# Performance work log

Measured on AMD Instinct MI355X. Metric: run time of the kernel, lower is better.

## Reference

```python
import jax, jax.numpy as jnp
import numpy as np

B, N, E = 4, 512, 128
NODE_F, EDGE_F, DYN_F, L = 16, 8, 6, 3
TOT_F = NODE_F + DYN_F  # 22


def setup_inputs() -> dict:
    key = jax.random.key(0)
    ks = jax.random.split(key, 20)
    s = 0.05
    return {
        "node_features": jax.random.normal(ks[0], (B, N, NODE_F), jnp.float32),
        "edge_features": jax.random.normal(ks[1], (B, N, N, EDGE_F), jnp.float32),
        "W": jax.random.normal(ks[2], (B, N, N), jnp.float32),
        "assigned": jax.random.randint(ks[3], (B, N), 0, 2) > 0,
        "open_group": jax.random.randint(ks[4], (B, N), 0, 2) > 0,
        "action_mask": jax.random.randint(ks[5], (B, N), 0, 2) > 0,
        "build_limit": jax.random.uniform(ks[6], (B, 3), jnp.float32, 0.5, 2.0),
        "open_group_size": jax.random.uniform(ks[7], (B, 3), jnp.float32, 0.0, 2.0),
        "node_embed_w": jax.random.normal(ks[8], (TOT_F, E), jnp.float32) * s,
        "node_embed_b": jnp.zeros((E,), jnp.float32),
        "mp_node_w": jax.random.normal(ks[9], (L, E, E), jnp.float32) * s,
        "mp_edge_w": jax.random.normal(ks[10], (L, EDGE_F, E), jnp.float32) * s,
        "mp_weight_w": jax.random.normal(ks[11], (L, E), jnp.float32) * s,
        "mp_out_w": jax.random.normal(ks[12], (L, E, E), jnp.float32) * s,
        "mp_out_b": jnp.zeros((L, E), jnp.float32),
        "context_w": jax.random.normal(ks[13], (E, E), jnp.float32) * s,
        "key_w": jax.random.normal(ks[14], (E, E), jnp.float32) * s,
        "logit_bias": jnp.zeros((1,), jnp.float32),
    }


def _policy_logits(node_features, edge_features, W, build_limit, open_group_size,
                   node_embed_w, node_embed_b, mp_node_w, mp_edge_w, mp_weight_w,
                   mp_out_w, mp_out_b, context_w, key_w, logit_bias,
                   assigned, open_group, action_mask):
    # --- dynamic node features: [B,N,6] ---
    ratio = open_group_size / jnp.maximum(build_limit, 1e-6)  # [B,3]
    dyn = jnp.concatenate([
        assigned.astype(jnp.float32)[..., None],
        open_group.astype(jnp.float32)[..., None],
        action_mask.astype(jnp.float32)[..., None],
        jnp.broadcast_to(ratio[:, None, :], (node_features.shape[0], node_features.shape[1], 3)),
    ], axis=-1)
    x = jnp.concatenate([node_features, dyn], axis=-1)  # [B,N,22]
    h = x @ node_embed_w + node_embed_b  # [B,N,E]

    # --- edge-aware message passing, residual per layer ---
    for l in range(L):
        hi = h @ mp_node_w[l]  # [B,N,E]
        ej = jnp.einsum('bijf,fe->bije', edge_features, mp_edge_w[l])  # [B,N,N,E]
        wij = W[..., None] * mp_weight_w[l]  # [B,N,N,E]
        msg = jnp.tanh(hi[:, :, None, :] + ej + wij)  # [B,N,N,E]
        agg = msg.mean(axis=2)  # [B,N,E]
        h = h + agg @ mp_out_w[l] + mp_out_b[l]

    # --- context attention logits ---
    og = open_group.astype(jnp.float32)
    has_open = jnp.any(open_group, axis=-1, keepdims=True)  # [B,1]
    denom = jnp.maximum(og.sum(axis=-1, keepdims=True), 1.0)  # [B,1]
    group_mean = (h * og[..., None]).sum(axis=1) / denom  # [B,E]
    sep_emb = h[:, 0, :]
    context = jnp.where(has_open, group_mean, sep_emb)  # [B,E]
    query = context @ context_w  # [B,E]
    keys = h @ key_w  # [B,N,E]
    logits = jnp.einsum('be,bne->bn', query, keys) / jnp.sqrt(jnp.float32(h.shape[-1]))
    logits = logits + logit_bias[0]
    logits = jnp.where(action_mask, logits, -1e9)
    return logits


def reference(node_features, edge_features, W, assigned, open_group, action_mask,
              build_limit, open_group_size, node_embed_w, node_embed_b,
              mp_node_w, mp_edge_w, mp_weight_w, mp_out_w, mp_out_b,
              context_w, key_w, logit_bias):
    return _policy_logits(node_features, edge_features, W, build_limit, open_group_size,
                          node_embed_w, node_embed_b, mp_node_w, mp_edge_w, mp_weight_w,
                          mp_out_w, mp_out_b, context_w, key_w, logit_bias,
                          assigned, open_group, action_mask)
```

## Files before the change

kernel.cpp:

```cpp
#include <hip/hip_runtime.h>
#include <math.h>

#define BB 4
#define NN 512
#define EE 128
#define NODE_F 16
#define EDGE_F 8
#define LL 3

typedef __attribute__((ext_vector_type(8))) short bf16x8;
typedef __attribute__((ext_vector_type(4))) float f32x4;

__device__ __forceinline__ ushort bf_hi(float x) {
    uint u = __float_as_uint(x);
    return (ushort)((u + 0x7fffu + ((u >> 16) & 1u)) >> 16);
}
__device__ __forceinline__ float bf_f(ushort h) {
    return __uint_as_float(((uint)h) << 16);
}

__global__ __launch_bounds__(512) void k_rows(
    const float* __restrict__ nf,
    const float* __restrict__ ef,
    const float* __restrict__ W,
    const int*   __restrict__ assigned,
    const int*   __restrict__ open_group,
    const int*   __restrict__ action_mask,
    const float* __restrict__ build_limit,
    const float* __restrict__ open_group_size,
    const float* __restrict__ embed_w,
    const float* __restrict__ embed_b,
    const float* __restrict__ node_w,
    const float* __restrict__ edge_w,
    const float* __restrict__ weight_w,
    const float* __restrict__ out_w,
    const float* __restrict__ out_b,
    float* __restrict__ hout)
{
    const int i   = blockIdx.x;
    const int b   = blockIdx.y;
    const int t   = threadIdx.x;
    const int l   = t & 63;
    const int w   = t >> 6;
    const int e   = t & 127;
    const int ks  = t >> 7;
    const int row = b * NN + i;

    __shared__ bf16x8 afr[32 * 64];
    __shared__ float hsh[EE];
    __shared__ float hipart[4][EE];
    __shared__ float opart[4][EE];
    __shared__ float aggfin[EE];
    __shared__ float xsh[24];

    if (t < NODE_F) {
        xsh[t] = nf[row * NODE_F + t];
    } else if (t == 16) {
        xsh[16] = assigned[row] ? 1.0f : 0.0f;
    } else if (t == 17) {
        xsh[17] = open_group[row] ? 1.0f : 0.0f;
    } else if (t == 18) {
        xsh[18] = action_mask[row] ? 1.0f : 0.0f;
    } else if (t < 22) {
        int k = t - 19;
        xsh[t] = open_group_size[b * 3 + k] / fmaxf(build_limit[b * 3 + k], 1e-6f);
    }

    {
        const float* efr = ef + (size_t)row * NN * EDGE_F;
        const float* Wr  = W + (size_t)row * NN;
        #pragma unroll
        for (int q = 0; q < 4; ++q) {
            const int eid = t + 512 * q;
            const int ll  = eid & 63;
            const int jt  = eid >> 6;
            const int g   = ll >> 4;
            const int jj  = jt * 16 + (ll & 15);
            bf16x8 frag;
            if (g < 3) {
                const float4 a = *(const float4*)&efr[jj * 8];
                const float4 c4 = *(const float4*)&efr[jj * 8 + 4];
                float v[8] = {a.x, a.y, a.z, a.w, c4.x, c4.y, c4.z, c4.w};
                if (g < 2) {
                    #pragma unroll
                    for (int m = 0; m < 8; ++m) frag[m] = (short)bf_hi(v[m]);
                } else {
                    #pragma unroll
                    for (int m = 0; m < 8; ++m) {
                        ushort h = bf_hi(v[m]);
                        frag[m] = (short)bf_hi(v[m] - bf_f(h));
                    }
                }
            } else {
                float wv = Wr[jj];
                ushort h = bf_hi(wv);
                ushort lo = bf_hi(wv - bf_f(h));
                frag = (bf16x8){(short)h, (short)h, (short)lo, 0, 0, 0, 0, 0};
            }
            afr[eid] = frag;
        }
    }
    __syncthreads();

    if (t < EE) {
        float h0 = embed_b[t];
        #pragma unroll
        for (int k = 0; k < 22; ++k)
            h0 = fmaf(xsh[k], embed_w[k * EE + t], h0);
        hsh[t] = h0;
    }

    const float c  = 2.8853900817779268f;
    const int  le  = l & 15;
    const int  g   = l >> 4;
    const int  eN  = w * 16 + le;

    for (int lay = 0; lay < LL; ++lay) {
        __syncthreads();

        {
            const float* nw = node_w + lay * EE * EE + ks * 32 * EE + e;
            float hp = 0.0f;
            #pragma unroll
            for (int kk = 0; kk < 2; ++kk) {
                float wreg[16];
                #pragma unroll
                for (int k2 = 0; k2 < 16; ++k2)
                    wreg[k2] = nw[(kk * 16 + k2) * EE];
                #pragma unroll
                for (int k2 = 0; k2 < 16; ++k2)
                    hp = fmaf(hsh[ks * 32 + kk * 16 + k2], wreg[k2], hp);
            }
            hipart[ks][e] = hp;
        }

        bf16x8 bfrag;
        if (g == 3) {
            float x = c * weight_w[lay * EE + eN];
            ushort h = bf_hi(x);
            ushort lo = bf_hi(x - bf_f(h));
            bfrag = (bf16x8){(short)h, (short)lo, (short)h, 0, 0, 0, 0, 0};
        } else {
            const float* ewp = edge_w + lay * EDGE_F * EE + eN;
            if (g == 1) {
                #pragma unroll
                for (int m = 0; m < 8; ++m) {
                    float x = c * ewp[m * EE];
                    ushort h = bf_hi(x);
                    bfrag[m] = (short)bf_hi(x - bf_f(h));
                }
            } else {
                #pragma unroll
                for (int m = 0; m < 8; ++m)
                    bfrag[m] = (short)bf_hi(c * ewp[m * EE]);
            }
        }
        __syncthreads();

        const float hq = c * ((hipart[0][eN] + hipart[1][eN])
                            + (hipart[2][eN] + hipart[3][eN]));
        const f32x4 cin = {hq, hq, hq, hq};

        f32x4 rsum = {0.0f, 0.0f, 0.0f, 0.0f};
        #pragma unroll 4
        for (int jt = 0; jt < 32; ++jt) {
            bf16x8 a = afr[jt * 64 + l];
            f32x4 acc = __builtin_amdgcn_mfma_f32_16x16x32_bf16(a, bfrag, cin, 0, 0, 0);
            #pragma unroll
            for (int r = 0; r < 4; ++r) {
                float ex = __builtin_amdgcn_exp2f(acc[r]);
                rsum[r] += __builtin_amdgcn_rcpf(ex + 1.0f);
            }
        }
        float s = (rsum[0] + rsum[1]) + (rsum[2] + rsum[3]);
        s += __shfl_xor(s, 16);
        s += __shfl_xor(s, 32);
        if (l < 16)
            aggfin[w * 16 + le] = 1.0f - s * (1.0f / 256.0f);
        __syncthreads();

        {
            const float* ow = out_w + lay * EE * EE + ks * 32 * EE + e;
            float op = 0.0f;
            #pragma unroll
            for (int kk = 0; kk < 2; ++kk) {
                float wreg[16];
                #pragma unroll
                for (int k2 = 0; k2 < 16; ++k2)
                    wreg[k2] = ow[(kk * 16 + k2) * EE];
                #pragma unroll
                for (int k2 = 0; k2 < 16; ++k2)
                    op = fmaf(aggfin[ks * 32 + kk * 16 + k2], wreg[k2], op);
            }
            opart[ks][e] = op;
        }
        __syncthreads();

        if (t < EE) {
            hsh[t] = hsh[t] + out_b[lay * EE + t]
                   + (opart[0][t] + opart[1][t]) + (opart[2][t] + opart[3][t]);
        }
    }

    __syncthreads();
    if (t < EE) hout[(size_t)row * EE + t] = hsh[t];
}

__global__ __launch_bounds__(1024) void k_ctx(
    const float* __restrict__ hbuf,
    const int*   __restrict__ open_group,
    const float* __restrict__ context_w,
    const float* __restrict__ key_w,
    float* __restrict__ qk)
{
    const int b = blockIdx.x;
    const int t = threadIdx.x;
    const int e = t & 127;
    const int s = t >> 7;

    __shared__ float gmsh[8][EE];
    __shared__ float cntsh[8];
    __shared__ float csh[EE];
    __shared__ float qsh[EE];

    const float* hb = hbuf + (size_t)b * NN * EE;

    float gm = 0.0f, cnt = 0.0f;
    const int n0 = s * 64;
    #pragma unroll 8
    for (int u = 0; u < 64; ++u) {
        const int n = n0 + u;
        const float m = (float)open_group[b * NN + n];
        gm = fmaf(m, hb[(size_t)n * EE + e], gm);
        cnt += m;
    }
    gmsh[s][e] = gm;
    if (e == 0) cntsh[s] = cnt;
    __syncthreads();

    if (s == 0) {
        float ca = 0.0f, ga = 0.0f;
        #pragma unroll
        for (int u = 0; u < 8; ++u) { ca += cntsh[u]; ga += gmsh[u][e]; }
        csh[e] = (ca > 0.0f) ? (ga / fmaxf(ca, 1.0f)) : hb[e];
    }
    __syncthreads();

    if (s == 0) {
        float q = 0.0f;
        #pragma unroll
        for (int kk = 0; kk < 8; ++kk) {
            float wreg[16];
            #pragma unroll
            for (int k2 = 0; k2 < 16; ++k2)
                wreg[k2] = context_w[(kk * 16 + k2) * EE + e];
            #pragma unroll
            for (int k2 = 0; k2 < 16; ++k2)
                q = fmaf(csh[kk * 16 + k2], wreg[k2], q);
        }
        qsh[e] = q;
    }
    __syncthreads();

    if (s == 0) {
        float acc = 0.0f;
        const float* kr = key_w + e * EE;
        #pragma unroll
        for (int kk = 0; kk < 8; ++kk) {
            float wreg[16];
            #pragma unroll
            for (int k2 = 0; k2 < 16; ++k2)
                wreg[k2] = kr[kk * 16 + k2];
            #pragma unroll
            for (int k2 = 0; k2 < 16; ++k2)
                acc = fmaf(wreg[k2], qsh[kk * 16 + k2], acc);
        }
        qk[b * EE + e] = acc;
    }
}

__global__ __launch_bounds__(512) void k_logits(
    const float* __restrict__ hbuf,
    const float* __restrict__ qk,
    const int*   __restrict__ action_mask,
    const float* __restrict__ logit_bias,
    float* __restrict__ out)
{
    const int b    = blockIdx.y;
    const int base = blockIdx.x * 32;
    const int wid  = threadIdx.x >> 6;
    const int lane = threadIdx.x & 63;

    const float* hb = hbuf + (size_t)b * NN * EE;
    const float* qb = qk + b * EE;
    const float q0 = qb[lane];
    const float q1 = qb[lane + 64];
    const float lb = logit_bias[0];

    #pragma unroll
    for (int u = 0; u < 4; ++u) {
        const int r = base + wid * 4 + u;
        const float* hr = hb + (size_t)r * EE;
        float p = hr[lane] * q0 + hr[lane + 64] * q1;
        #pragma unroll
        for (int off = 32; off; off >>= 1)
            p += __shfl_down(p, off);
        if (lane == 0) {
            float v = fmaf(p, 0.08838834764831845f, lb);
            out[b * NN + r] = action_mask[b * NN + r] ? v : -1000000000.0f;
        }
    }
}

extern "C" void kernel_launch(void* const* d_in, const int* in_sizes, int n_in,
                              void* d_out, int out_size, void* d_ws, size_t ws_size,
                              hipStream_t stream) {
    const float* nf         = (const float*)d_in[0];
    const float* ef         = (const float*)d_in[1];
    const float* W          = (const float*)d_in[2];
    const int*   assigned   = (const int*)d_in[3];
    const int*   open_group = (const int*)d_in[4];
    const int*   action_mask= (const int*)d_in[5];
    const float* build_limit= (const float*)d_in[6];
    const float* og_size    = (const float*)d_in[7];
    const float* embed_w    = (const float*)d_in[8];
    const float* embed_b    = (const float*)d_in[9];
    const float* node_w     = (const float*)d_in[10];
    const float* edge_w     = (const float*)d_in[11];
    const float* weight_w   = (const float*)d_in[12];
    const float* out_w      = (const float*)d_in[13];
    const float* out_b      = (const float*)d_in[14];
    const float* context_w  = (const float*)d_in[15];
    const float* key_w      = (const float*)d_in[16];
    const float* logit_bias = (const float*)d_in[17];

    float* hbuf = (float*)d_ws;
    float* qk   = hbuf + (size_t)BB * NN * EE;

    dim3 grid_rows(NN, BB, 1);
    k_rows<<<grid_rows, 512, 0, stream>>>(nf, ef, W, assigned, open_group,
        action_mask, build_limit, og_size, embed_w, embed_b, node_w, edge_w,
        weight_w, out_w, out_b, hbuf);

    k_ctx<<<BB, 1024, 0, stream>>>(hbuf, open_group, context_w, key_w, qk);

    dim3 grid_log(16, BB, 1);
    k_logits<<<grid_log, 512, 0, stream>>>(hbuf, qk, action_mask, logit_bias,
        (float*)d_out);
}
```

Baseline: 231.7 us.

## Replace shared-memory partial sums with wave shuffles and fuse group-mean via atomics

Inside k_rows, the per-layer node and out projections are remapped so each wave reduces its K-slices with xor shuffles instead of writing partials to shared memory. This removes two block-wide barriers per layer. The open-group mean is now accumulated with global atomics at the end of k_rows, so k_ctx shrinks to a 128-thread kernel that no longer rescans hbuf. A small zeroing kernel is added for the accumulators. Float atomics make the group sum order nondeterministic, and the new layout changes how the weight reads coalesce.

```diff
diff --git a/kernel.cpp b/kernel.cpp
--- a/kernel.cpp
+++ b/kernel.cpp
@@ -17,6 +17,11 @@
 }
 __device__ __forceinline__ float bf_f(ushort h) {
     return __uint_as_float(((uint)h) << 16);
+}
+
+__global__ __launch_bounds__(512) void k_zero(float* __restrict__ gbuf) {
+    for (int i = threadIdx.x; i < BB * EE + BB; i += 512)
+        gbuf[i] = 0.0f;
 }
 
 __global__ __launch_bounds__(512) void k_rows(
@@ -35,21 +40,19 @@
     const float* __restrict__ weight_w,
     const float* __restrict__ out_w,
     const float* __restrict__ out_b,
-    float* __restrict__ hout)
+    float* __restrict__ hout,
+    float* __restrict__ gsum,
+    float* __restrict__ gcnt)
 {
     const int i   = blockIdx.x;
     const int b   = blockIdx.y;
     const int t   = threadIdx.x;
     const int l   = t & 63;
     const int w   = t >> 6;
-    const int e   = t & 127;
-    const int ks  = t >> 7;
     const int row = b * NN + i;
 
     __shared__ bf16x8 afr[32 * 64];
     __shared__ float hsh[EE];
-    __shared__ float hipart[4][EE];
-    __shared__ float opart[4][EE];
     __shared__ float aggfin[EE];
     __shared__ float xsh[24];
 
@@ -118,9 +121,9 @@
     for (int lay = 0; lay < LL; ++lay) {
         __syncthreads();
 
+        float hp = 0.0f;
         {
-            const float* nw = node_w + lay * EE * EE + ks * 32 * EE + e;
-            float hp = 0.0f;
+            const float* nw = node_w + lay * EE * EE + g * 32 * EE + eN;
             #pragma unroll
             for (int kk = 0; kk < 2; ++kk) {
                 float wreg[16];
@@ -129,10 +132,12 @@
                     wreg[k2] = nw[(kk * 16 + k2) * EE];
                 #pragma unroll
                 for (int k2 = 0; k2 < 16; ++k2)
-                    hp = fmaf(hsh[ks * 32 + kk * 16 + k2], wreg[k2], hp);
-            }
-            hipart[ks][e] = hp;
-        }
+                    hp = fmaf(hsh[g * 32 + kk * 16 + k2], wreg[k2], hp);
+            }
+            hp += __shfl_xor(hp, 16);
+            hp += __shfl_xor(hp, 32);
+        }
+        const float hq = c * hp;
 
         bf16x8 bfrag;
         if (g == 3) {
@@ -155,10 +160,7 @@
                     bfrag[m] = (short)bf_hi(c * ewp[m * EE]);
             }
         }
-        __syncthreads();
-
-        const float hq = c * ((hipart[0][eN] + hipart[1][eN])
-                            + (hipart[2][eN] + hipart[3][eN]));
+
         const f32x4 cin = {hq, hq, hq, hq};
 
         f32x4 rsum = {0.0f, 0.0f, 0.0f, 0.0f};
@@ -176,12 +178,12 @@
         s += __shfl_xor(s, 16);
         s += __shfl_xor(s, 32);
         if (l < 16)
-            aggfin[w * 16 + le] = 1.0f - s * (1.0f / 256.0f);
+            aggfin[eN] = 1.0f - s * (1.0f / 256.0f);
         __syncthreads();
 
+        float op = 0.0f;
         {
-            const float* ow = out_w + lay * EE * EE + ks * 32 * EE + e;
-            float op = 0.0f;
+            const float* ow = out_w + lay * EE * EE + g * 32 * EE + eN;
             #pragma unroll
             for (int kk = 0; kk < 2; ++kk) {
                 float wreg[16];
@@ -190,93 +192,71 @@
                     wreg[k2] = ow[(kk * 16 + k2) * EE];
                 #pragma unroll
                 for (int k2 = 0; k2 < 16; ++k2)
-                    op = fmaf(aggfin[ks * 32 + kk * 16 + k2], wreg[k2], op);
-            }
-            opart[ks][e] = op;
-        }
-        __syncthreads();
-
-        if (t < EE) {
-            hsh[t] = hsh[t] + out_b[lay * EE + t]
-                   + (opart[0][t] + opart[1][t]) + (opart[2][t] + opart[3][t]);
-        }
+                    op = fmaf(aggfin[g * 32 + kk * 16 + k2], wreg[k2], op);
+            }
+            op += __shfl_xor(op, 16);
+            op += __shfl_xor(op, 32);
+        }
+        if (l < 16)
+            hsh[eN] = hsh[eN] + out_b[lay * EE + eN] + op;
     }
 
     __syncthreads();
-    if (t < EE) hout[(size_t)row * EE + t] = hsh[t];
-}
-
-__global__ __launch_bounds__(1024) void k_ctx(
+    if (t < EE) {
+        const float hv = hsh[t];
+        hout[(size_t)row * EE + t] = hv;
+        if (open_group[row]) atomicAdd(&gsum[b * EE + t], hv);
+    }
+    if (t == 256 && open_group[row]) atomicAdd(&gcnt[b], 1.0f);
+}
+
+__global__ __launch_bounds__(128) void k_ctx(
     const float* __restrict__ hbuf,
-    const int*   __restrict__ open_group,
+    const float* __restrict__ gsum,
+    const float* __restrict__ gcnt,
     const float* __restrict__ context_w,
     const float* __restrict__ key_w,
     float* __restrict__ qk)
 {
     const int b = blockIdx.x;
-    const int t = threadIdx.x;
-    const int e = t & 127;
-    const int s = t >> 7;
-
-    __shared__ float gmsh[8][EE];
-    __shared__ float cntsh[8];
+    const int e = threadIdx.x;
+
     __shared__ float csh[EE];
     __shared__ float qsh[EE];
 
-    const float* hb = hbuf + (size_t)b * NN * EE;
-
-    float gm = 0.0f, cnt = 0.0f;
-    const int n0 = s * 64;
-    #pragma unroll 8
-    for (int u = 0; u < 64; ++u) {
-        const int n = n0 + u;
-        const float m = (float)open_group[b * NN + n];
-        gm = fmaf(m, hb[(size_t)n * EE + e], gm);
-        cnt += m;
-    }
-    gmsh[s][e] = gm;
-    if (e == 0) cntsh[s] = cnt;
+    const float cnt = gcnt[b];
+    const float ctx = (cnt > 0.0f) ? (gsum[b * EE + e] / fmaxf(cnt, 1.0f))
+                                   : hbuf[(size_t)b * NN * EE + e];
+    csh[e] = ctx;
     __syncthreads();
 
-    if (s == 0) {
-        float ca = 0.0f, ga = 0.0f;
-        #pragma unroll
-        for (int u = 0; u < 8; ++u) { ca += cntsh[u]; ga += gmsh[u][e]; }
-        csh[e] = (ca > 0.0f) ? (ga / fmaxf(ca, 1.0f)) : hb[e];
-    }
+    float q = 0.0f;
+    #pragma unroll
+    for (int kk = 0; kk < 8; ++kk) {
+        float wreg[16];
+        #pragma unroll
+        for (int k2 = 0; k2 < 16; ++k2)
+            wreg[k2] = context_w[(kk * 16 + k2) * EE + e];
+        #pragma unroll
+        for (int k2 = 0; k2 < 16; ++k2)
+            q = fmaf(csh[kk * 16 + k2], wreg[k2], q);
+    }
+    qsh[e] = q;
     __syncthreads();
 
-    if (s == 0) {
-        float q = 0.0f;
-        #pragma unroll
-        for (int kk = 0; kk < 8; ++kk) {
-            float wreg[16];
-            #pragma unroll
-            for (int k2 = 0; k2 < 16; ++k2)
-                wreg[k2] = context_w[(kk * 16 + k2) * EE + e];
-            #pragma unroll
-            for (int k2 = 0; k2 < 16; ++k2)
-                q = fmaf(csh[kk * 16 + k2], wreg[k2], q);
-        }
-        qsh[e] = q;
-    }
-    __syncthreads();
-
-    if (s == 0) {
-        float acc = 0.0f;
-        const float* kr = key_w + e * EE;
-        #pragma unroll
-        for (int kk = 0; kk < 8; ++kk) {
-            float wreg[16];
-            #pragma unroll
-            for (int k2 = 0; k2 < 16; ++k2)
-                wreg[k2] = kr[kk * 16 + k2];
-            #pragma unroll
-            for (int k2 = 0; k2 < 16; ++k2)
-                acc = fmaf(wreg[k2], qsh[kk * 16 + k2], acc);
-        }
-        qk[b * EE + e] = acc;
-    }
+    float acc = 0.0f;
+    const float* kr = key_w + e * EE;
+    #pragma unroll
+    for (int kk = 0; kk < 8; ++kk) {
+        float wreg[16];
+        #pragma unroll
+        for (int k2 = 0; k2 < 16; ++k2)
+            wreg[k2] = kr[kk * 16 + k2];
+        #pragma unroll
+        for (int k2 = 0; k2 < 16; ++k2)
+            acc = fmaf(wreg[k2], qsh[kk * 16 + k2], acc);
+    }
+    qk[b * EE + e] = acc;
 }
 
 __global__ __launch_bounds__(512) void k_logits(
@@ -336,13 +316,18 @@
 
     float* hbuf = (float*)d_ws;
     float* qk   = hbuf + (size_t)BB * NN * EE;
+    float* gbuf = qk + BB * EE;
+    float* gsum = gbuf;
+    float* gcnt = gbuf + BB * EE;
+
+    k_zero<<<1, 512, 0, stream>>>(gbuf);
 
     dim3 grid_rows(NN, BB, 1);
     k_rows<<<grid_rows, 512, 0, stream>>>(nf, ef, W, assigned, open_group,
         action_mask, build_limit, og_size, embed_w, embed_b, node_w, edge_w,
-        weight_w, out_w, out_b, hbuf);
-
-    k_ctx<<<BB, 1024, 0, stream>>>(hbuf, open_group, context_w, key_w, qk);
+        weight_w, out_w, out_b, hbuf, gsum, gcnt);
+
+    k_ctx<<<BB, 128, 0, stream>>>(hbuf, gsum, gcnt, context_w, key_w, qk);
 
     dim3 grid_log(16, BB, 1);
     k_logits<<<grid_log, 512, 0, stream>>>(hbuf, qk, action_mask, logit_bias,
```

Measured after the change: 220.9 us. -4.7%, faster.
